# Kernel optimization log

Measured on AMD Instinct MI355X. Metric: run time of the kernel, lower is better.

The kernel has to match this reference:

```python
import jax, jax.numpy as jnp
import numpy as np

# ---- Config constants (from DGM Config) ----
DIM = 20        # number of assets; inputs have DIM+1 cols (last is time)
DELTA = 0.01    # finite-difference step / covariance scale
RHO = 0.5       # asset correlation
MC = 32         # Config.mc_num
N = 2048        # interior points (inputs holds 2*N rows)
UNITS = 128     # Config.unit_num
LAYERS = 3      # Config.layer_num
SIG = 0.2       # Config._sig
MU = 0.05       # Config._mu
R = 0.05        # Config._r

_cov = DELTA * (np.full((DIM, DIM), RHO, dtype=np.float64) + (1.0 - RHO) * np.eye(DIM))
L_TRIL = jnp.asarray(np.linalg.cholesky(_cov).astype(np.float32))  # (DIM, DIM) lower-tri


def setup_inputs() -> dict:
    key = jax.random.key(0)
    ks = jax.random.split(key, 20)
    d = DIM + 1
    u = lambda k, shp: jax.random.uniform(k, shp, jnp.float32, -0.05, 0.05)
    inp = {
        # strictly positive inputs so boundary prod**(1/DIM) is well-defined
        "inputs": jax.random.uniform(ks[0], (2 * N, d), jnp.float32, 0.1, 1.0),
        "eps": jax.random.normal(ks[1], (MC, N, DIM), jnp.float32),
        "w1": u(ks[2], (d, UNITS)), "b1": u(ks[3], (UNITS,)),
        "uzl": u(ks[4], (d, UNITS)), "wzl": u(ks[5], (UNITS, UNITS)), "bzl": u(ks[6], (UNITS,)),
        "ugl": u(ks[7], (d, UNITS)), "wgl": u(ks[8], (UNITS, UNITS)), "bgl": u(ks[9], (UNITS,)),
        "url": u(ks[10], (d, UNITS)), "wrl": u(ks[11], (UNITS, UNITS)), "brl": u(ks[12], (UNITS,)),
        "uhl": u(ks[13], (d, UNITS)), "whl": u(ks[14], (UNITS, UNITS)), "bhl": u(ks[15], (UNITS,)),
        "w": u(ks[16], (UNITS, 1)), "b": u(ks[17], (1,)),
    }
    return inp


def _value(x, w1, b1, uzl, wzl, bzl, ugl, wgl, bgl, url, wrl, brl, uhl, whl, bhl, w, b):
    # DGM gated residual network; x: (..., DIM+1) -> (..., 1)
    act = jnp.tanh
    s = act(x @ w1 + b1)
    for _ in range(LAYERS):
        z = act(x @ uzl + s @ wzl + bzl)
        g = act(x @ ugl + s @ wgl + bgl)
        r = act(x @ url + s @ wrl + brl)
        h = act(x @ uhl + (s * r) @ whl + bhl)
        s = (1.0 - g) * h + z * s
    return s @ w + b


def reference(inputs, eps, w1, b1, uzl, wzl, bzl, ugl, wgl, bgl, url, wrl, brl,
              uhl, whl, bhl, w, b):
    params = (w1, b1, uzl, wzl, bzl, ugl, wgl, bgl, url, wrl, brl, uhl, whl, bhl, w, b)
    val = lambda x: _value(x, *params)
    x1, x2 = jnp.split(inputs, 2, axis=0)          # interior / boundary points

    # first-order grad of value w.r.t. interior inputs
    fprime = jax.grad(lambda x: val(x).sum())(x1)  # (N, DIM+1)
    drift = jnp.concatenate([MU * x1[:, :-1], jnp.ones((x1.shape[0], 1), x1.dtype)], axis=1)
    term1_1 = jnp.sum(drift * fprime, axis=1)      # (N,)

    # correlated MVN perturbations (reparameterized): loc + eps @ L^T
    loc = x1[:, :-1]                               # (N, DIM)
    sample = loc[None, :, :] + jnp.einsum('mnd,kd->mnk', eps, L_TRIL)  # (MC, N, DIM)
    xdiff = sample * (SIG * loc)[None, :, :]
    violation = jnp.concatenate([xdiff, jnp.zeros((MC, x1.shape[0], 1), x1.dtype)], axis=2)
    xplus = x1[None, :, :] + violation             # (MC, N, DIM+1)

    fprime_plus = jax.grad(lambda x: val(x).sum())(xplus)  # (MC, N, DIM+1)
    term1_2 = jnp.sum(
        jnp.mean((fprime_plus - fprime[None, :, :]) / DELTA * violation, axis=0), axis=1)

    # boundary residual: value - payoff (geometric-mean call payoff)
    payoff = jax.nn.relu(jnp.power(jnp.prod(x2[:, :-1], axis=1), 1.0 / DIM))
    term2 = jnp.squeeze(val(x2), -1) - payoff

    interior = term1_1 + 0.5 * term1_2 - R * jnp.squeeze(val(x1), -1)
    return jnp.concatenate([interior, term2], axis=0)  # (2N,)
```

## Files before the change

kernel.cpp:

```cpp
#include <hip/hip_runtime.h>
#include <math.h>

#define DIMN 20
#define DD 21
#define NN 2048
#define MCN 32
#define UNITS 128
#define SIGC 0.2f
#define MUC 0.05f
#define RC 0.05f
#define DELTAC 0.01f

#define TM 32
#define PTOT (NN + MCN*NN + NN)
#define NBLK (PTOT/TM)

#define OFF_L 0
#define OFF_WT 512
#define OFF_UZGR (OFF_WT + 4*16384)
#define OFF_WZGR (OFF_UZGR + 8192)
#define OFF_FP1  (OFF_WZGR + 49152)
#define OFF_VAL1 (OFF_FP1 + NN*DD)
#define OFF_VAL2 (OFF_VAL1 + NN)
#define OFF_T12  (OFF_VAL2 + NN)
#define OFF_GATES (OFF_T12 + NN)

#define ST_S1 0
#define ST_Z1 4096
#define ST_G1 8192
#define ST_R1 12288
#define ST_Z2 16384
#define ST_G2 20480
#define ST_R2 24576
#define GB_STRIDE 28672

#define L_TOT_SG 17728
#define L_TOT_RC 21824

#define ELT44(...) _Pragma("unroll") for (int p = 0; p < 4; p++){ _Pragma("unroll") for (int jj = 0; jj < 4; jj++){ __VA_ARGS__; } }

__device__ __forceinline__ int offq(int row, int p0){
    return row*32 + ((p0 + 4*(row&7)) & 31);
}
__device__ __forceinline__ int offs(int row, int p){
    return row*32 + (((p & 28) + 4*(row&7)) & 31) + (p & 3);
}

__device__ __forceinline__ float ftanh(float x){
    float cx = fminf(9.f, fmaxf(-9.f, x));
    float e  = __expf(2.f*cx);
    return fmaf(-2.f, __builtin_amdgcn_rcpf(e + 1.f), 1.f);
}

#define FMA16(acc, s4, w4) \
  acc[0][0]=fmaf(s4.x,w4.x,acc[0][0]); acc[0][1]=fmaf(s4.x,w4.y,acc[0][1]); \
  acc[0][2]=fmaf(s4.x,w4.z,acc[0][2]); acc[0][3]=fmaf(s4.x,w4.w,acc[0][3]); \
  acc[1][0]=fmaf(s4.y,w4.x,acc[1][0]); acc[1][1]=fmaf(s4.y,w4.y,acc[1][1]); \
  acc[1][2]=fmaf(s4.y,w4.z,acc[1][2]); acc[1][3]=fmaf(s4.y,w4.w,acc[1][3]); \
  acc[2][0]=fmaf(s4.z,w4.x,acc[2][0]); acc[2][1]=fmaf(s4.z,w4.y,acc[2][1]); \
  acc[2][2]=fmaf(s4.z,w4.z,acc[2][2]); acc[2][3]=fmaf(s4.z,w4.w,acc[2][3]); \
  acc[3][0]=fmaf(s4.w,w4.x,acc[3][0]); acc[3][1]=fmaf(s4.w,w4.y,acc[3][1]); \
  acc[3][2]=fmaf(s4.w,w4.z,acc[3][2]); acc[3][3]=fmaf(s4.w,w4.w,acc[3][3]);

__device__ __forceinline__ void mm_d(const float* __restrict__ gW, int K,
    const float* __restrict__ vec, float acc[4][4], int jg, int p0)
{
    const float* wp = gW + 4*jg;
    __builtin_amdgcn_s_setprio(1);
    #pragma unroll 8
    for (int k = 0; k < K; k++){
        float4 w4 = *(const float4*)(wp + k*UNITS);
        float4 s4 = *(const float4*)(vec + offq(k, p0));
        FMA16(acc, s4, w4)
    }
    __builtin_amdgcn_s_setprio(0);
}
__device__ __forceinline__ void mm2_d(const float* __restrict__ gWa, const float* __restrict__ gWb,
    int K, const float* __restrict__ vecA, const float* __restrict__ vecB,
    float acc[4][4], int jg, int p0)
{
    const float* wpa = gWa + 4*jg;
    const float* wpb = gWb + 4*jg;
    __builtin_amdgcn_s_setprio(1);
    #pragma unroll 4
    for (int k = 0; k < K; k++){
        float4 wa = *(const float4*)(wpa + k*UNITS);
        float4 sa = *(const float4*)(vecA + offq(k, p0));
        float4 wb = *(const float4*)(wpb + k*UNITS);
        float4 sb = *(const float4*)(vecB + offq(k, p0));
        FMA16(acc, sa, wa)
        FMA16(acc, sb, wb)
    }
    __builtin_amdgcn_s_setprio(0);
}
__device__ __forceinline__ void mm3_d(const float* __restrict__ gW, int K,
    const float* __restrict__ vec, float a0[4][4], float a1[4][4], float a2[4][4],
    int jg, int p0)
{
    const float* wp = gW + 4*jg;
    __builtin_amdgcn_s_setprio(1);
    #pragma unroll 4
    for (int k = 0; k < K; k++){
        const float* r = wp + k*384;
        float4 s4 = *(const float4*)(vec + offq(k, p0));
        float4 w0 = *(const float4*)(r);
        float4 w1v = *(const float4*)(r + 128);
        float4 w2 = *(const float4*)(r + 256);
        FMA16(a0, s4, w0) FMA16(a1, s4, w1v) FMA16(a2, s4, w2)
    }
    __builtin_amdgcn_s_setprio(0);
}

__device__ __forceinline__ void write_own(float* buf, const float v[4][4], int j0, int p0){
    #pragma unroll
    for (int jj = 0; jj < 4; jj++){
        int j = j0 + jj;
        float4 q = make_float4(v[0][jj], v[1][jj], v[2][jj], v[3][jj]);
        *(float4*)(buf + offq(j, p0)) = q;
    }
}
__device__ __forceinline__ void read_own(const float* buf, float v[4][4], int j0, int p0){
    #pragma unroll
    for (int jj = 0; jj < 4; jj++){
        int j = j0 + jj;
        float4 q = *(const float4*)(buf + offq(j, p0));
        v[0][jj]=q.x; v[1][jj]=q.y; v[2][jj]=q.z; v[3][jj]=q.w;
    }
}
__device__ __forceinline__ void stash_w(float* buf, const float v[4][4], int t){
    #pragma unroll
    for (int jj = 0; jj < 4; jj++)
        *(float4*)(buf + (jj*256 + t)*4) = make_float4(v[0][jj], v[1][jj], v[2][jj], v[3][jj]);
}
__device__ __forceinline__ void stash_r(const float* buf, float v[4][4], int t){
    #pragma unroll
    for (int jj = 0; jj < 4; jj++){
        float4 q = *(const float4*)(buf + (jj*256 + t)*4);
        v[0][jj]=q.x; v[1][jj]=q.y; v[2][jj]=q.z; v[3][jj]=q.w;
    }
}

__device__ __forceinline__ void gate_f(const float* __restrict__ U, const float* __restrict__ W,
    const float* __restrict__ bias, const float* __restrict__ xT, const float* __restrict__ Sin,
    float out[4][4], int jg, int p0, int j0)
{
    float acc[4][4];
    float4 b = *(const float4*)(bias + j0);
    #pragma unroll
    for (int p = 0; p < 4; p++){ acc[p][0]=b.x; acc[p][1]=b.y; acc[p][2]=b.z; acc[p][3]=b.w; }
    mm_d(U, DD, xT, acc, jg, p0);
    mm_d(W, UNITS, Sin, acc, jg, p0);
    #pragma unroll
    for (int p = 0; p < 4; p++)
        #pragma unroll
        for (int jj = 0; jj < 4; jj++) out[p][jj] = ftanh(acc[p][jj]);
}

__device__ __forceinline__ void gate3_f(const float* __restrict__ Uzgr, const float* __restrict__ Wzgr,
    const float* __restrict__ bz, const float* __restrict__ bg, const float* __restrict__ br,
    const float* __restrict__ xT, const float* __restrict__ Sin,
    float zt[4][4], float gt[4][4], float rt[4][4],
    int jg, int p0, int j0)
{
    float4 b0 = *(const float4*)(bz + j0);
    float4 b1 = *(const float4*)(bg + j0);
    float4 b2 = *(const float4*)(br + j0);
    #pragma unroll
    for (int p = 0; p < 4; p++){
        zt[p][0]=b0.x; zt[p][1]=b0.y; zt[p][2]=b0.z; zt[p][3]=b0.w;
        gt[p][0]=b1.x; gt[p][1]=b1.y; gt[p][2]=b1.z; gt[p][3]=b1.w;
        rt[p][0]=b2.x; rt[p][1]=b2.y; rt[p][2]=b2.z; rt[p][3]=b2.w;
    }
    mm3_d(Uzgr, DD, xT, zt, gt, rt, jg, p0);
    mm3_d(Wzgr, UNITS, Sin, zt, gt, rt, jg, p0);
    ELT44(zt[p][jj]=ftanh(zt[p][jj]); gt[p][jj]=ftanh(gt[p][jj]); rt[p][jj]=ftanh(rt[p][jj]))
}

__global__ void chol_kernel(float* __restrict__ Lout)
{
    if (threadIdx.x == 0 && blockIdx.x == 0) {
        const double beta = 0.01 * 0.5;
        const double diag = 0.01;
        double c[DIMN], d[DIMN];
        double S = 0.0;
        for (int j = 0; j < DIMN; j++){
            double dj = sqrt(diag - S);
            double cj = (beta - S) / dj;
            d[j] = dj; c[j] = cj;
            S += cj*cj;
        }
        for (int i = 0; i < DIMN; i++)
            for (int j = 0; j < DIMN; j++)
                Lout[i*DIMN + j] = (j < i) ? (float)c[j] : (j == i) ? (float)d[i] : 0.0f;
    }
}

__global__ void transpose_k(const float* __restrict__ wz, const float* __restrict__ wg,
                            const float* __restrict__ wr, const float* __restrict__ wh,
                            float* __restrict__ WT)
{
    int idx = blockIdx.x*256 + threadIdx.x;
    int q = idx >> 14, r2 = idx & 16383, k = r2 >> 7, j = r2 & 127;
    const float* src = (q==0)? wz : (q==1)? wg : (q==2)? wr : wh;
    WT[(q<<14) + j*UNITS + k] = src[k*UNITS + j];
}

__global__ void pack_zgr(const float* __restrict__ uz, const float* __restrict__ ug,
                         const float* __restrict__ ur,
                         const float* __restrict__ wz, const float* __restrict__ wg,
                         const float* __restrict__ wr,
                         float* __restrict__ Uzgr, float* __restrict__ Wzgr)
{
    int idx = blockIdx.x*256 + threadIdx.x;
    if (idx < 128*384){
        int k = idx/384, c = idx - k*384, g = c >> 7, j = c & 127;
        const float* s = (g==0)? wz : (g==1)? wg : wr;
        Wzgr[idx] = s[k*UNITS + j];
        return;
    }
    int i2 = idx - 128*384;
    if (i2 < 21*384){
        int k = i2/384, c = i2 - k*384, g = c >> 7, j = c & 127;
        const float* s = (g==0)? uz : (g==1)? ug : ur;
        Uzgr[i2] = s[k*UNITS + j];
    }
}

#define DGM_PARAMS \
    const float* __restrict__ inputs, const float* __restrict__ eps, \
    const float* __restrict__ w1, const float* __restrict__ b1, \
    const float* __restrict__ uz, const float* __restrict__ bz, \
    const float* __restrict__ ug, const float* __restrict__ bg, \
    const float* __restrict__ ur, const float* __restrict__ br, \
    const float* __restrict__ uh, const float* __restrict__ wh, const float* __restrict__ bh, \
    const float* __restrict__ wv, const float* __restrict__ bv, \
    const float* __restrict__ Lm, const float* __restrict__ WT, \
    const float* __restrict__ Uzgr, const float* __restrict__ Wzgr, \
    float* __restrict__ gws, \
    float* __restrict__ fp1, float* __restrict__ val1, float* __restrict__ val2, \
    float* __restrict__ t12acc

#define DGM_ARGS inputs, eps, w1, b1, uz, bz, ug, bg, ur, br, uh, wh, bh, wv, bv, \
    Lm, WT, Uzgr, Wzgr, gws, fp1, val1, val2, t12acc

template<int SG>
__device__ __forceinline__ void dgm_body(float* lds, DGM_PARAMS)
{
    float* S0  = lds;
    float* S1  = SG ? lds : lds + 4096;
    float* S2  = lds + (SG ? 4096 : 8192);
    float* Db  = lds + (SG ? 8192 : 12288);
    float* Db2 = lds + (SG ? 12288 : 16384);
    float* xT  = lds + (SG ? 16384 : 20480);
    float* Vb  = lds + (SG ? 17056 : 21152);

    const int t  = threadIdx.x;
    const int jg = t & 31;
    const int pg = t >> 5;
    const int p0 = pg * 4;
    const int j0 = jg * 4;
    const int P0 = blockIdx.x * TM;
    const int type = (P0 < NN) ? 0 : (P0 < NN + MCN*NN) ? 1 : 2;
    int base_n = 0, mrow = 0;
    if (type == 1){ int q = P0 - NN; mrow = q >> 11; base_n = q & (NN-1); }

    float* gb = gws + (size_t)blockIdx.x * GB_STRIDE;

    {
        int p = t & 31, kq = t >> 5;
        for (int ki = 0; ki < 3; ki++){
            int k = kq + 8*ki;
            if (k > DIMN) break;
            float xv;
            if (type == 0){
                xv = inputs[(P0 + p)*DD + k];
            } else if (type == 2){
                xv = inputs[(NN + (P0 - NN - MCN*NN) + p)*DD + k];
            } else {
                int n = base_n + p;
                float x1v = inputs[n*DD + k];
                if (k == DIMN) xv = x1v;
                else {
                    const float* ep = eps + (size_t)(mrow*NN + n)*DIMN;
                    float a = x1v;
                    for (int d = 0; d < DIMN; d++) a = fmaf(ep[d], Lm[k*DIMN + d], a);
                    float viol = a * (SIGC * x1v);
                    Vb[offs(k, p)] = viol;
                    xv = x1v + viol;
                }
            }
            xT[offs(k, p)] = xv;
        }
    }
    __syncthreads();

    float s_own[4][4];
    {
        float acc[4][4];
        float4 b = *(const float4*)(b1 + j0);
        #pragma unroll
        for (int p = 0; p < 4; p++){ acc[p][0]=b.x; acc[p][1]=b.y; acc[p][2]=b.z; acc[p][3]=b.w; }
        mm_d(w1, DD, xT, acc, jg, p0);
        ELT44(s_own[p][jj] = ftanh(acc[p][jj]))
        write_own(S0, s_own, j0, p0);
        __syncthreads();
    }

    float zt[4][4], gt[4][4], rt[4][4], ht[4][4];

#define GATES(SIN, SMUL) \
    gate3_f(Uzgr, Wzgr, bz, bg, br, xT, SIN, zt, gt, rt, jg, p0, j0); \
    __syncthreads(); \
    { float tt[4][4]; ELT44(tt[p][jj] = SMUL[p][jj]*rt[p][jj]) write_own(Db, tt, j0, p0); } \
    __syncthreads(); \
    gate_f(uh, wh, bh, xT, Db, ht, jg, p0, j0);

#define FWD_LAYER(SIN) \
    GATES(SIN, s_own) \
    ELT44(s_own[p][jj] = (1.f - gt[p][jj])*ht[p][jj] + zt[p][jj]*s_own[p][jj])

    FWD_LAYER(S0)
    if (SG){ if (type != 2){
        stash_w(gb + ST_S1, s_own, t);
        stash_w(gb + ST_Z1, zt, t); stash_w(gb + ST_G1, gt, t); stash_w(gb + ST_R1, rt, t);
    } }
    else   { write_own(S1, s_own, j0, p0); }
    __syncthreads();
    write_own(Db, s_own, j0, p0);
    __syncthreads();

    FWD_LAYER(Db)
    if (SG && type != 2){
        stash_w(gb + ST_Z2, zt, t); stash_w(gb + ST_G2, gt, t); stash_w(gb + ST_R2, rt, t);
    }
    write_own(S2, s_own, j0, p0);
    __syncthreads();

    FWD_LAYER(S2)

    {
        float4 wv4 = *(const float4*)(wv + j0);
        float vs[4];
        #pragma unroll
        for (int p = 0; p < 4; p++)
            vs[p] = s_own[p][0]*wv4.x + s_own[p][1]*wv4.y + s_own[p][2]*wv4.z + s_own[p][3]*wv4.w;
        __syncthreads();
        *(float4*)(Db + jg*32 + p0) = make_float4(vs[0], vs[1], vs[2], vs[3]);
        __syncthreads();
        if (t < TM){
            float v = bv[0];
            for (int j2 = 0; j2 < 32; j2++) v += Db[j2*32 + t];
            if (type == 0) val1[P0 + t] = v;
            else if (type == 2) val2[P0 + t - NN - MCN*NN] = v;
        }
        __syncthreads();
    }
    if (type == 2) return;

    float ds[4][4];
    {
        float4 wv4 = *(const float4*)(wv + j0);
        #pragma unroll
        for (int p = 0; p < 4; p++){ ds[p][0]=wv4.x; ds[p][1]=wv4.y; ds[p][2]=wv4.z; ds[p][3]=wv4.w; }
    }
    float proj[4] = {0.f, 0.f, 0.f, 0.f};
    float dxp[3] = {0.f, 0.f, 0.f};
    const int pi = t >> 3, il = t & 7;

    const float* WTz = WT;
    const float* WTg = WT + 16384;
    const float* WTr = WT + 2*16384;
    const float* WTh = WT + 3*16384;

#define DX_DOT(UMAT, BUF) \
    { _Pragma("unroll") for (int ii = 0; ii < 3; ii++){ \
        int i = il + 8*ii; \
        if (i < DD){ \
            const float* Urow = UMAT + i*UNITS; \
            float a = 0.f; \
            for (int j2 = 0; j2 < UNITS; j2++) a = fmaf(BUF[offs(j2, pi)], Urow[j2], a); \
            dxp[ii] += a; \
        } } }

#define PROJ_D(UMAT, SEL) \
    { float uv[4][4]; \
      ELT44(uv[p][jj] = 0.f) \
      mm_d(UMAT, DIMN, Vb, uv, jg, p0); \
      ELT44(proj[p] += uv[p][jj]*SEL[p][jj]) }

#define BWD_LAYER(SLP, MODE, GZ, GG, GR) \
    { \
    float dsn[4][4], dhp[4][4]; \
    if (MODE == 1){ \
        float slg[4][4]; read_own(SLP, slg, j0, p0); \
        GATES(SLP, slg) \
    } \
    {  \
        float sl[4][4], zv[4][4], gv[4][4], hv[4][4]; \
        if (MODE == 2){ stash_r(gb + ST_S1, sl, t); stash_r(gb + GZ, zv, t); stash_r(gb + GG, gv, t); } \
        else if (MODE == 3){ read_own(SLP, sl, j0, p0); stash_r(gb + GZ, zv, t); stash_r(gb + GG, gv, t); } \
        else if (MODE == 0){ read_own(S2, sl, j0, p0); ELT44(zv[p][jj]=zt[p][jj]; gv[p][jj]=gt[p][jj]; hv[p][jj]=ht[p][jj]) } \
        else { read_own(SLP, sl, j0, p0); ELT44(zv[p][jj]=zt[p][jj]; gv[p][jj]=gt[p][jj]; hv[p][jj]=ht[p][jj]) } \
        if (MODE == 2 || MODE == 3){ \
            float sn[4][4]; \
            if (MODE == 2){ read_own(S2, sn, j0, p0); } \
            else { stash_r(gb + ST_S1, sn, t); } \
            ELT44(hv[p][jj] = (sn[p][jj] - zv[p][jj]*sl[p][jj]) / (1.f - gv[p][jj])) \
        } \
        float dzp[4][4], dgp[4][4]; \
        ELT44(float d=ds[p][jj]; float zz=zv[p][jj]; \
            dzp[p][jj] = d*sl[p][jj]*(1.f - zz*zz); dsn[p][jj] = d*zz) \
        ELT44(float d=ds[p][jj]; float gg=gv[p][jj]; float hh=hv[p][jj]; \
            dgp[p][jj] = -d*hh*(1.f - gg*gg); \
            dhp[p][jj] = d*(1.f - gg)*(1.f - hh*hh)) \
        __syncthreads(); \
        write_own(Db,  dzp, j0, p0); \
        write_own(Db2, dgp, j0, p0); \
        __syncthreads(); \
        if (type == 1){ PROJ_D(uz, dzp) PROJ_D(ug, dgp) } \
        else { DX_DOT(uz, Db) DX_DOT(ug, Db2) } \
    } \
    mm2_d(WTz, WTg, UNITS, Db, Db2, dsn, jg, p0); \
     \
    __syncthreads(); \
    write_own(Db, dhp, j0, p0); \
    __syncthreads(); \
    if (type == 1){ PROJ_D(uh, dhp) } else { DX_DOT(uh, Db) } \
    float dsr[4][4]; \
    ELT44(dsr[p][jj] = 0.f) \
    mm_d(WTh, UNITS, Db, dsr, jg, p0); \
    {  \
        float rv[4][4], sl[4][4], drp[4][4]; \
        if (MODE == 2){ stash_r(gb + GR, rv, t); stash_r(gb + ST_S1, sl, t); } \
        else if (MODE == 3){ stash_r(gb + GR, rv, t); read_own(SLP, sl, j0, p0); } \
        else if (MODE == 0){ ELT44(rv[p][jj] = rt[p][jj]) read_own(S2, sl, j0, p0); } \
        else { ELT44(rv[p][jj] = rt[p][jj]) read_own(SLP, sl, j0, p0); } \
        ELT44(float dr=dsr[p][jj]; float rr=rv[p][jj]; \
            drp[p][jj] = dr*sl[p][jj]*(1.f - rr*rr); dsn[p][jj] += dr*rr) \
        __syncthreads(); \
        write_own(Db, drp, j0, p0); \
        __syncthreads(); \
        if (type == 1){ PROJ_D(ur, drp) } else { DX_DOT(ur, Db) } \
    } \
    mm_d(WTr, UNITS, Db, dsn, jg, p0); \
    ELT44(ds[p][jj] = dsn[p][jj]) \
    }

    BWD_LAYER(S0, 0, ST_Z2, ST_G2, ST_R2)
    BWD_LAYER(S1, (SG ? 2 : 1), ST_Z2, ST_G2, ST_R2)
    if (SG){ BWD_LAYER(S0, 3, ST_Z1, ST_G1, ST_R1) }
    else   { BWD_LAYER(S0, 1, ST_Z1, ST_G1, ST_R1) }

    {
        float s0l[4][4];
        read_own(S0, s0l, j0, p0);
        float v0[4][4];
        ELT44(v0[p][jj] = ds[p][jj]*(1.f - s0l[p][jj]*s0l[p][jj]))

        if (type == 1){
            PROJ_D(w1, v0)
            __syncthreads();
            *(float4*)(Db + jg*32 + p0) = make_float4(proj[0], proj[1], proj[2], proj[3]);
            __syncthreads();
            if (t < TM){
                float s = 0.f;
                for (int j2 = 0; j2 < 32; j2++) s += Db[j2*32 + t];
                atomicAdd(t12acc + base_n + t, s);
            }
        } else {
            __syncthreads();
            write_own(Db, v0, j0, p0);
            __syncthreads();
            DX_DOT(w1, Db)
            #pragma unroll
            for (int ii = 0; ii < 3; ii++){
                int i = il + 8*ii;
                if (i < DD) fp1[(P0 + pi)*DD + i] = dxp[ii];
            }
        }
    }
}

__global__ __launch_bounds__(256) __attribute__((amdgpu_waves_per_eu(2,2))) void dgm_sg(DGM_PARAMS){
    __shared__ float lds[L_TOT_SG];
    dgm_body<1>(lds, DGM_ARGS);
}
__global__ __launch_bounds__(256) __attribute__((amdgpu_waves_per_eu(2,2))) void dgm_rc(DGM_PARAMS){
    __shared__ float lds[L_TOT_RC];
    dgm_body<0>(lds, DGM_ARGS);
}

__global__ void finalize_k(const float* __restrict__ inputs, const float* __restrict__ eps,
    const float* __restrict__ Lm, const float* __restrict__ fp1, const float* __restrict__ val1,
    const float* __restrict__ val2, const float* __restrict__ t12acc, float* __restrict__ out)
{
    int n = blockIdx.x*256 + threadIdx.x;
    if (n >= NN) return;
    float fp[DD];
    #pragma unroll
    for (int k = 0; k < DD; k++) fp[k] = fp1[n*DD + k];
    float t11 = fp[DIMN];
    #pragma unroll
    for (int k = 0; k < DIMN; k++) t11 = fmaf(MUC*inputs[n*DD + k], fp[k], t11);
    float esum[DIMN];
    #pragma unroll
    for (int d = 0; d < DIMN; d++){
        float a = 0.f;
        for (int m = 0; m < MCN; m++) a += eps[(size_t)(m*NN + n)*DIMN + d];
        esum[d] = a;
    }
    float t12b = 0.f;
    #pragma unroll
    for (int k = 0; k < DIMN; k++){
        float loc = inputs[n*DD + k];
        float ssum = (float)MCN * loc;
        #pragma unroll
        for (int d = 0; d < DIMN; d++) ssum = fmaf(esum[d], Lm[k*DIMN + d], ssum);
        float vsum = ssum * (SIGC*loc);
        t12b = fmaf(fp[k], vsum, t12b);
    }
    float term12 = (t12acc[n] - t12b) * (1.0f/(DELTAC*(float)MCN));
    out[n] = t11 + 0.5f*term12 - RC*val1[n];

    float prod = 1.f;
    #pragma unroll
    for (int k = 0; k < DIMN; k++) prod *= inputs[(NN + n)*DD + k];
    float payoff = powf(prod, 1.0f/(float)DIMN);
    if (!(payoff > 0.f)) payoff = 0.f;
    out[NN + n] = val2[n] - payoff;
}

extern "C" void kernel_launch(void* const* d_in, const int* in_sizes, int n_in,
                              void* d_out, int out_size, void* d_ws, size_t ws_size,
                              hipStream_t stream)
{
    const float* inputs = (const float*)d_in[0];
    const float* eps    = (const float*)d_in[1];
    const float* w1     = (const float*)d_in[2];
    const float* b1     = (const float*)d_in[3];
    const float* uz     = (const float*)d_in[4];
    const float* wz     = (const float*)d_in[5];
    const float* bz     = (const float*)d_in[6];
    const float* ug     = (const float*)d_in[7];
    const float* wg     = (const float*)d_in[8];
    const float* bg     = (const float*)d_in[9];
    const float* urr    = (const float*)d_in[10];
    const float* wr     = (const float*)d_in[11];
    const float* br     = (const float*)d_in[12];
    const float* uh     = (const float*)d_in[13];
    const float* wh     = (const float*)d_in[14];
    const float* bh     = (const float*)d_in[15];
    const float* wv     = (const float*)d_in[16];
    const float* bv     = (const float*)d_in[17];

    float* ws    = (float*)d_ws;
    float* Lm    = ws + OFF_L;
    float* WT    = ws + OFF_WT;
    float* Uzgr  = ws + OFF_UZGR;
    float* Wzgr  = ws + OFF_WZGR;
    float* fp1   = ws + OFF_FP1;
    float* val1  = ws + OFF_VAL1;
    float* val2  = ws + OFF_VAL2;
    float* t12   = ws + OFF_T12;
    float* gates = ws + OFF_GATES;
    float* out   = (float*)d_out;

    hipMemsetAsync(t12, 0, NN*sizeof(float), stream);
    hipLaunchKernelGGL(chol_kernel, dim3(1), dim3(64), 0, stream, Lm);
    hipLaunchKernelGGL(transpose_k, dim3(256), dim3(256), 0, stream, wz, wg, wr, wh, WT);
    hipLaunchKernelGGL(pack_zgr, dim3(224), dim3(256), 0, stream, uz, ug, urr, wz, wg, wr, Uzgr, Wzgr);

    size_t need_bytes = ((size_t)OFF_GATES + (size_t)NBLK * (size_t)GB_STRIDE) * sizeof(float);
    if (ws_size >= need_bytes){
        hipLaunchKernelGGL(dgm_sg, dim3(NBLK), dim3(256), 0, stream,
            inputs, eps, w1, b1, uz, bz, ug, bg, urr, br, uh, wh, bh, wv, bv,
            Lm, WT, Uzgr, Wzgr, gates, fp1, val1, val2, t12);
    } else {
        hipLaunchKernelGGL(dgm_rc, dim3(NBLK), dim3(256), 0, stream,
            inputs, eps, w1, b1, uz, bz, ug, bg, urr, br, uh, wh, bh, wv, bv,
            Lm, WT, Uzgr, Wzgr, gates, fp1, val1, val2, t12);
    }
    hipLaunchKernelGGL(finalize_k, dim3(8), dim3(256), 0, stream,
        inputs, eps, Lm, fp1, val1, val2, t12, out);
}
```

Measured before the change: 1.230 ms.

## Fuse h-gate backward matmul with z/g matmul using third LDS buffer

Adds a third LDS delta buffer so the h-gate gradient is written together with the z and g gradients. The three W^T matmuls then run in one fused loop, which removes a sync pair and a separate pass over the LDS vectors. In the SG variant, S0 aliases the buffer Db3 now occupies, so the first-layer state is recomputed from the inputs into S2 before the last backward layer. This costs more LDS in the RC variant, which may lower occupancy, and adds a small recompute matmul.

After: 1.254 ms, median of 2. 1.02x slower.

```diff
diff --git a/kernel.cpp b/kernel.cpp
--- a/kernel.cpp
+++ b/kernel.cpp
@@ -35,7 +35,7 @@
 #define GB_STRIDE 28672
 
 #define L_TOT_SG 17728
-#define L_TOT_RC 21824
+#define L_TOT_RC 25920
 
 #define ELT44(...) _Pragma("unroll") for (int p = 0; p < 4; p++){ _Pragma("unroll") for (int jj = 0; jj < 4; jj++){ __VA_ARGS__; } }
 
@@ -75,21 +75,26 @@
     }
     __builtin_amdgcn_s_setprio(0);
 }
-__device__ __forceinline__ void mm2_d(const float* __restrict__ gWa, const float* __restrict__ gWb,
-    int K, const float* __restrict__ vecA, const float* __restrict__ vecB,
-    float acc[4][4], int jg, int p0)
+__device__ __forceinline__ void mm3w_d(const float* __restrict__ gWa, const float* __restrict__ gWb,
+    const float* __restrict__ gWc, int K,
+    const float* __restrict__ vecA, const float* __restrict__ vecB, const float* __restrict__ vecC,
+    float accAB[4][4], float accC[4][4], int jg, int p0)
 {
     const float* wpa = gWa + 4*jg;
     const float* wpb = gWb + 4*jg;
+    const float* wpc = gWc + 4*jg;
     __builtin_amdgcn_s_setprio(1);
-    #pragma unroll 4
+    #pragma unroll 2
     for (int k = 0; k < K; k++){
         float4 wa = *(const float4*)(wpa + k*UNITS);
         float4 sa = *(const float4*)(vecA + offq(k, p0));
         float4 wb = *(const float4*)(wpb + k*UNITS);
         float4 sb = *(const float4*)(vecB + offq(k, p0));
-        FMA16(acc, sa, wa)
-        FMA16(acc, sb, wb)
+        float4 wc = *(const float4*)(wpc + k*UNITS);
+        float4 sc = *(const float4*)(vecC + offq(k, p0));
+        FMA16(accAB, sa, wa)
+        FMA16(accAB, sb, wb)
+        FMA16(accC,  sc, wc)
     }
     __builtin_amdgcn_s_setprio(0);
 }
@@ -251,8 +256,9 @@
     float* S2  = lds + (SG ? 4096 : 8192);
     float* Db  = lds + (SG ? 8192 : 12288);
     float* Db2 = lds + (SG ? 12288 : 16384);
-    float* xT  = lds + (SG ? 16384 : 20480);
-    float* Vb  = lds + (SG ? 17056 : 21152);
+    float* Db3 = SG ? lds : lds + 20480;
+    float* xT  = lds + (SG ? 16384 : 24576);
+    float* Vb  = lds + (SG ? 17056 : 25248);
 
     const int t  = threadIdx.x;
     const int jg = t & 31;
@@ -390,7 +396,7 @@
 
 #define BWD_LAYER(SLP, MODE, GZ, GG, GR) \
     { \
-    float dsn[4][4], dhp[4][4]; \
+    float dsn[4][4], dsr[4][4]; \
     if (MODE == 1){ \
         float slg[4][4]; read_own(SLP, slg, j0, p0); \
         GATES(SLP, slg) \
@@ -407,7 +413,7 @@
             else { stash_r(gb + ST_S1, sn, t); } \
             ELT44(hv[p][jj] = (sn[p][jj] - zv[p][jj]*sl[p][jj]) / (1.f - gv[p][jj])) \
         } \
-        float dzp[4][4], dgp[4][4]; \
+        float dzp[4][4], dgp[4][4], dhp[4][4]; \
         ELT44(float d=ds[p][jj]; float zz=zv[p][jj]; \
             dzp[p][jj] = d*sl[p][jj]*(1.f - zz*zz); dsn[p][jj] = d*zz) \
         ELT44(float d=ds[p][jj]; float gg=gv[p][jj]; float hh=hv[p][jj]; \
@@ -416,27 +422,21 @@
         __syncthreads(); \
         write_own(Db,  dzp, j0, p0); \
         write_own(Db2, dgp, j0, p0); \
+        write_own(Db3, dhp, j0, p0); \
         __syncthreads(); \
-        if (type == 1){ PROJ_D(uz, dzp) PROJ_D(ug, dgp) } \
-        else { DX_DOT(uz, Db) DX_DOT(ug, Db2) } \
+        if (type == 1){ PROJ_D(uz, dzp) PROJ_D(ug, dgp) PROJ_D(uh, dhp) } \
+        else { DX_DOT(uz, Db) DX_DOT(ug, Db2) DX_DOT(uh, Db3) } \
+        ELT44(dsr[p][jj] = 0.f) \
+        mm3w_d(WTz, WTg, WTh, UNITS, Db, Db2, Db3, dsn, dsr, jg, p0); \
     } \
-    mm2_d(WTz, WTg, UNITS, Db, Db2, dsn, jg, p0); \
-     \
-    __syncthreads(); \
-    write_own(Db, dhp, j0, p0); \
-    __syncthreads(); \
-    if (type == 1){ PROJ_D(uh, dhp) } else { DX_DOT(uh, Db) } \
-    float dsr[4][4]; \
-    ELT44(dsr[p][jj] = 0.f) \
-    mm_d(WTh, UNITS, Db, dsr, jg, p0); \
     {  \
-        float rv[4][4], sl[4][4], drp[4][4]; \
-        if (MODE == 2){ stash_r(gb + GR, rv, t); stash_r(gb + ST_S1, sl, t); } \
-        else if (MODE == 3){ stash_r(gb + GR, rv, t); read_own(SLP, sl, j0, p0); } \
-        else if (MODE == 0){ ELT44(rv[p][jj] = rt[p][jj]) read_own(S2, sl, j0, p0); } \
-        else { ELT44(rv[p][jj] = rt[p][jj]) read_own(SLP, sl, j0, p0); } \
+        float rv[4][4], sl2[4][4], drp[4][4]; \
+        if (MODE == 2){ stash_r(gb + GR, rv, t); stash_r(gb + ST_S1, sl2, t); } \
+        else if (MODE == 3){ stash_r(gb + GR, rv, t); read_own(SLP, sl2, j0, p0); } \
+        else if (MODE == 0){ ELT44(rv[p][jj] = rt[p][jj]) read_own(S2, sl2, j0, p0); } \
+        else { ELT44(rv[p][jj] = rt[p][jj]) read_own(SLP, sl2, j0, p0); } \
         ELT44(float dr=dsr[p][jj]; float rr=rv[p][jj]; \
-            drp[p][jj] = dr*sl[p][jj]*(1.f - rr*rr); dsn[p][jj] += dr*rr) \
+            drp[p][jj] = dr*sl2[p][jj]*(1.f - rr*rr); dsn[p][jj] += dr*rr) \
         __syncthreads(); \
         write_own(Db, drp, j0, p0); \
         __syncthreads(); \
@@ -446,14 +446,27 @@
     ELT44(ds[p][jj] = dsn[p][jj]) \
     }
 
-    BWD_LAYER(S0, 0, ST_Z2, ST_G2, ST_R2)
+    BWD_LAYER(S2, 0, ST_Z2, ST_G2, ST_R2)
     BWD_LAYER(S1, (SG ? 2 : 1), ST_Z2, ST_G2, ST_R2)
-    if (SG){ BWD_LAYER(S0, 3, ST_Z1, ST_G1, ST_R1) }
-    else   { BWD_LAYER(S0, 1, ST_Z1, ST_G1, ST_R1) }
+    if (SG){
+        float acc[4][4];
+        float4 b = *(const float4*)(b1 + j0);
+        #pragma unroll
+        for (int p = 0; p < 4; p++){ acc[p][0]=b.x; acc[p][1]=b.y; acc[p][2]=b.z; acc[p][3]=b.w; }
+        mm_d(w1, DD, xT, acc, jg, p0);
+        float s0r[4][4];
+        ELT44(s0r[p][jj] = ftanh(acc[p][jj]))
+        __syncthreads();
+        write_own(S2, s0r, j0, p0);
+        __syncthreads();
+        BWD_LAYER(S2, 3, ST_Z1, ST_G1, ST_R1)
+    } else {
+        BWD_LAYER(S0, 1, ST_Z1, ST_G1, ST_R1)
+    }
 
     {
         float s0l[4][4];
-        read_own(S0, s0l, j0, p0);
+        read_own((SG ? S2 : S0), s0l, j0, p0);
         float v0[4][4];
         ELT44(v0[p][jj] = ds[p][jj]*(1.f - s0l[p][jj]*s0l[p][jj]))
 
```
